# Kernel optimization log

Measured on AMD Instinct MI355X. Metric: run time of the kernel, lower is better.

Reference implementation:

```python
import jax, jax.numpy as jnp
import numpy as np


def setup_inputs() -> dict:
    key = jax.random.key(0)
    kq, kk, kv = jax.random.split(key, 3)
    B, N, M, H, D = 4, 2048, 2048, 8, 64
    queries = jax.random.normal(kq, (B, N, H, D), dtype=jnp.float32)
    keys = jax.random.normal(kk, (B, M, H, D), dtype=jnp.float32)
    values = jax.random.normal(kv, (B, M, H, D), dtype=jnp.float32)
    return {"queries": queries, "keys": keys, "values": values}


def reference(queries, keys, values):
    # queries: [B,N,H,D], keys/values: [B,M,H,D]
    D = queries.shape[3]
    softmax_temp = 1.0 / (D ** 0.5)
    QK = jnp.einsum('bnhd,bmhd->bnmh', queries, keys)  # [B,N,M,H]
    A = jax.nn.softmax(softmax_temp * QK, axis=2)      # softmax over M
    queried_values = jnp.einsum('bnmh,bmhd->bnhd', A, values)
    attention_weight = jnp.transpose(A, (0, 3, 1, 2))  # [B,H,N,M]
    return (queried_values, attention_weight)
```

## Files before the change

kernel.cpp:

```cpp
#include <hip/hip_runtime.h>

typedef __bf16 bf16x8 __attribute__((ext_vector_type(8)));
typedef float floatx4 __attribute__((ext_vector_type(4)));
typedef unsigned short ushort8 __attribute__((ext_vector_type(8)));
typedef unsigned short ushort4v __attribute__((ext_vector_type(4)));

#define MFMA(a, b, c) __builtin_amdgcn_mfma_f32_16x16x32_bf16((a), (b), (c), 0, 0, 0)

__device__ __forceinline__ unsigned short f2bf(float x) {
  union { float f; unsigned u; } v; v.f = x;
  unsigned r = v.u + 0x7FFFu + ((v.u >> 16) & 1u);
  return (unsigned short)(r >> 16);
}

__global__ __launch_bounds__(256)
void prep(const float* __restrict__ K, const float* __restrict__ V,
          unsigned short* __restrict__ Kb, unsigned short* __restrict__ Vt)
{
  int id = blockIdx.x * 256 + threadIdx.x;
  int isV = id >> 19;
  int cch = id & 524287;
  int bh = cch >> 14;
  int mt = (cch >> 9) & 31;
  int g  = cch & 511;
  int r  = g >> 3;
  int s  = g & 7;
  int e8 = s ^ (r & 7);
  int b = bh >> 3, h = bh & 7;
  ushort8 o;
  if (!isV) {
    const float* p = K + (((size_t)(b * 2048 + mt * 64 + r) * 8 + h) * 64 + e8 * 8);
    float4 x0 = *(const float4*)p;
    float4 x1 = *(const float4*)(p + 4);
    o[0] = f2bf(x0.x); o[1] = f2bf(x0.y); o[2] = f2bf(x0.z); o[3] = f2bf(x0.w);
    o[4] = f2bf(x1.x); o[5] = f2bf(x1.y); o[6] = f2bf(x1.z); o[7] = f2bf(x1.w);
    *(ushort8*)(Kb + (size_t)cch * 8) = o;
  } else {
    const float* p = V + (((size_t)(b * 2048 + mt * 64 + e8 * 8) * 8 + h) * 64 + r);
    #pragma unroll
    for (int j = 0; j < 8; ++j) o[j] = f2bf(p[(size_t)j * 512]);
    *(ushort8*)(Vt + (size_t)cch * 8) = o;
  }
}

__device__ __forceinline__ void stage2k(const unsigned short* gsrc, unsigned short* lds,
                                        int w, int l)
{
  const char* g = (const char*)gsrc + w * 2048 + l * 16;
  char* sd = (char*)lds + w * 2048;
  __builtin_amdgcn_global_load_lds((const __attribute__((address_space(1))) unsigned int*)g,
                                   (__attribute__((address_space(3))) unsigned int*)sd, 16, 0, 0);
  __builtin_amdgcn_global_load_lds((const __attribute__((address_space(1))) unsigned int*)(g + 1024),
                                   (__attribute__((address_space(3))) unsigned int*)(sd + 1024), 16, 0, 0);
}

__device__ __forceinline__ bf16x8 frag(const unsigned short* lds, int r, int bo)
{
  int slot = ((bo >> 4) ^ r) & 7;
  return *(const bf16x8*)((const char*)lds + r * 128 + (slot << 4));
}

__global__ __launch_bounds__(256, 4)
void attn_fwd(const float* __restrict__ Q, const unsigned short* __restrict__ Kb,
              const unsigned short* __restrict__ Vt,
              float* __restrict__ outQV, float* __restrict__ outA)
{
  __shared__ __align__(16) unsigned short Ks[2][4096];
  __shared__ __align__(16) unsigned short Vs[2][4096];
  __shared__ __align__(16) unsigned short As[4096];

  const int tid = threadIdx.x;
  const int w  = tid >> 6;
  const int l  = tid & 63;
  const int c  = l & 15;
  const int q4 = l >> 4;

  const int bx = blockIdx.x;
  const int qt = bx & 31;
  const int h  = (bx >> 5) & 7;
  const int b  = bx >> 8;
  const int q0 = qt * 64;

  const float scale = 0.125f * 1.44269504088896340736f;

  const size_t base = (size_t)b * (2048 * 512) + (size_t)h * 64;
  const float* Qb = Q + base + (size_t)q0 * 512;

  const unsigned short* Kt0 = Kb + (size_t)(b * 8 + h) * (32 * 4096);
  const unsigned short* Vt0 = Vt + (size_t)(b * 8 + h) * (32 * 4096);

  bf16x8 bQ0, bQ1;
  {
    const float* qp = Qb + (size_t)(16 * w + c) * 512 + q4 * 8;
    float4 qa0 = *(const float4*)(qp);
    float4 qa1 = *(const float4*)(qp + 4);
    float4 qb0 = *(const float4*)(qp + 32);
    float4 qb1 = *(const float4*)(qp + 36);
    ushort8 t0, t1;
    t0[0]=f2bf(qa0.x*scale); t0[1]=f2bf(qa0.y*scale); t0[2]=f2bf(qa0.z*scale); t0[3]=f2bf(qa0.w*scale);
    t0[4]=f2bf(qa1.x*scale); t0[5]=f2bf(qa1.y*scale); t0[6]=f2bf(qa1.z*scale); t0[7]=f2bf(qa1.w*scale);
    t1[0]=f2bf(qb0.x*scale); t1[1]=f2bf(qb0.y*scale); t1[2]=f2bf(qb0.z*scale); t1[3]=f2bf(qb0.w*scale);
    t1[4]=f2bf(qb1.x*scale); t1[5]=f2bf(qb1.y*scale); t1[6]=f2bf(qb1.z*scale); t1[7]=f2bf(qb1.w*scale);
    bQ0 = __builtin_bit_cast(bf16x8, t0);
    bQ1 = __builtin_bit_cast(bf16x8, t1);
  }

  stage2k(Kt0, Ks[0], w, l);
  float lsum[4] = {0.f, 0.f, 0.f, 0.f};
  int cur = 0;
  for (int mt = 0; mt < 32; ++mt) {
    __syncthreads();
    if (mt + 1 < 32) stage2k(Kt0 + (size_t)(mt + 1) * 4096, Ks[cur ^ 1], w, l);
    const unsigned short* Kc = Ks[cur];
    #pragma unroll
    for (int t = 0; t < 4; ++t) {
      bf16x8 aK0 = frag(Kc, t * 16 + c, q4 * 16);
      bf16x8 aK1 = frag(Kc, t * 16 + c, 64 + q4 * 16);
      floatx4 acc = {0.f, 0.f, 0.f, 0.f};
      acc = MFMA(aK0, bQ0, acc);
      acc = MFMA(aK1, bQ1, acc);
      #pragma unroll
      for (int i = 0; i < 4; ++i) lsum[i] += __builtin_amdgcn_exp2f(acc[i]);
    }
    cur ^= 1;
  }
  float rs = (lsum[0] + lsum[1]) + (lsum[2] + lsum[3]);
  rs += __shfl_xor(rs, 16);
  rs += __shfl_xor(rs, 32);
  const float rcp = 1.0f / rs;

  floatx4 Oacc[4];
  #pragma unroll
  for (int t = 0; t < 4; ++t) Oacc[t] = (floatx4){0.f, 0.f, 0.f, 0.f};

  const int arow = 16 * w + c;
  float* aRowP = outA + (((size_t)(b * 8 + h) * 2048 + q0 + arow) * 2048) + q4 * 4;

  __syncthreads();
  stage2k(Kt0, Ks[0], w, l);
  stage2k(Vt0, Vs[0], w, l);
  cur = 0;
  for (int mt = 0; mt < 32; ++mt) {
    __syncthreads();
    if (mt + 1 < 32) {
      stage2k(Kt0 + (size_t)(mt + 1) * 4096, Ks[cur ^ 1], w, l);
      stage2k(Vt0 + (size_t)(mt + 1) * 4096, Vs[cur ^ 1], w, l);
    }
    const unsigned short* Kc = Ks[cur];
    const unsigned short* Vc = Vs[cur];
    const int mc = mt * 64;
    #pragma unroll
    for (int t = 0; t < 4; ++t) {
      bf16x8 aK0 = frag(Kc, t * 16 + c, q4 * 16);
      bf16x8 aK1 = frag(Kc, t * 16 + c, 64 + q4 * 16);
      floatx4 acc = {0.f, 0.f, 0.f, 0.f};
      acc = MFMA(aK0, bQ0, acc);
      acc = MFMA(aK1, bQ1, acc);
      floatx4 av;
      av[0] = __builtin_amdgcn_exp2f(acc[0]) * rcp;
      av[1] = __builtin_amdgcn_exp2f(acc[1]) * rcp;
      av[2] = __builtin_amdgcn_exp2f(acc[2]) * rcp;
      av[3] = __builtin_amdgcn_exp2f(acc[3]) * rcp;
      __builtin_nontemporal_store(av, (floatx4*)(aRowP + mc + t * 16));
      ushort4v us = { f2bf(av[0]), f2bf(av[1]), f2bf(av[2]), f2bf(av[3]) };
      int bo = t * 32 + q4 * 8;
      int slot = ((bo >> 4) ^ arow) & 7;
      *(ushort4v*)((char*)As + arow * 128 + (slot << 4) + (bo & 15)) = us;
    }
    bf16x8 aP0 = frag(As, arow, q4 * 16);
    bf16x8 aP1 = frag(As, arow, 64 + q4 * 16);
    #pragma unroll
    for (int t = 0; t < 4; ++t) {
      bf16x8 bV0 = frag(Vc, t * 16 + c, q4 * 16);
      bf16x8 bV1 = frag(Vc, t * 16 + c, 64 + q4 * 16);
      Oacc[t] = MFMA(aP0, bV0, Oacc[t]);
      Oacc[t] = MFMA(aP1, bV1, Oacc[t]);
    }
    cur ^= 1;
  }

  #pragma unroll
  for (int t = 0; t < 4; ++t) {
    #pragma unroll
    for (int i = 0; i < 4; ++i) {
      outQV[base + (size_t)(q0 + 16 * w + q4 * 4 + i) * 512 + t * 16 + c] = Oacc[t][i];
    }
  }
}

extern "C" void kernel_launch(void* const* d_in, const int* in_sizes, int n_in,
                              void* d_out, int out_size, void* d_ws, size_t ws_size,
                              hipStream_t stream)
{
  const float* Q = (const float*)d_in[0];
  const float* K = (const float*)d_in[1];
  const float* V = (const float*)d_in[2];
  float* outQV = (float*)d_out;
  float* outA  = (float*)d_out + 4194304;

  unsigned short* Kb = (unsigned short*)d_ws;
  unsigned short* Vt = (unsigned short*)d_ws + 4194304;

  prep<<<dim3(4096), dim3(256), 0, stream>>>(K, V, Kb, Vt);
  attn_fwd<<<dim3(1024), dim3(256), 0, stream>>>(Q, Kb, Vt, outQV, outA);
}
```

Baseline: 656.2 us.

## Read K/V fragments straight from global memory and remap blocks for XCD locality

```diff
diff --git a/kernel.cpp b/kernel.cpp
--- a/kernel.cpp
+++ b/kernel.cpp
@@ -25,39 +25,26 @@
   int g  = cch & 511;
   int r  = g >> 3;
   int s  = g & 7;
-  int e8 = s ^ (r & 7);
   int b = bh >> 3, h = bh & 7;
   ushort8 o;
   if (!isV) {
-    const float* p = K + (((size_t)(b * 2048 + mt * 64 + r) * 8 + h) * 64 + e8 * 8);
+    const float* p = K + (((size_t)(b * 2048 + mt * 64 + r) * 8 + h) * 64 + s * 8);
     float4 x0 = *(const float4*)p;
     float4 x1 = *(const float4*)(p + 4);
     o[0] = f2bf(x0.x); o[1] = f2bf(x0.y); o[2] = f2bf(x0.z); o[3] = f2bf(x0.w);
     o[4] = f2bf(x1.x); o[5] = f2bf(x1.y); o[6] = f2bf(x1.z); o[7] = f2bf(x1.w);
     *(ushort8*)(Kb + (size_t)cch * 8) = o;
   } else {
-    const float* p = V + (((size_t)(b * 2048 + mt * 64 + e8 * 8) * 8 + h) * 64 + r);
+    const float* p = V + (((size_t)(b * 2048 + mt * 64 + s * 8) * 8 + h) * 64 + r);
     #pragma unroll
     for (int j = 0; j < 8; ++j) o[j] = f2bf(p[(size_t)j * 512]);
     *(ushort8*)(Vt + (size_t)cch * 8) = o;
   }
 }
 
-__device__ __forceinline__ void stage2k(const unsigned short* gsrc, unsigned short* lds,
-                                        int w, int l)
+__device__ __forceinline__ bf16x8 gfrag(const unsigned short* tile, int r, int e)
 {
-  const char* g = (const char*)gsrc + w * 2048 + l * 16;
-  char* sd = (char*)lds + w * 2048;
-  __builtin_amdgcn_global_load_lds((const __attribute__((address_space(1))) unsigned int*)g,
-                                   (__attribute__((address_space(3))) unsigned int*)sd, 16, 0, 0);
-  __builtin_amdgcn_global_load_lds((const __attribute__((address_space(1))) unsigned int*)(g + 1024),
-                                   (__attribute__((address_space(3))) unsigned int*)(sd + 1024), 16, 0, 0);
-}
-
-__device__ __forceinline__ bf16x8 frag(const unsigned short* lds, int r, int bo)
-{
-  int slot = ((bo >> 4) ^ r) & 7;
-  return *(const bf16x8*)((const char*)lds + r * 128 + (slot << 4));
+  return *(const bf16x8*)(tile + r * 64 + e);
 }
 
 __global__ __launch_bounds__(256, 4)
@@ -65,8 +52,6 @@
               const unsigned short* __restrict__ Vt,
               float* __restrict__ outQV, float* __restrict__ outA)
 {
-  __shared__ __align__(16) unsigned short Ks[2][4096];
-  __shared__ __align__(16) unsigned short Vs[2][4096];
   __shared__ __align__(16) unsigned short As[4096];
 
   const int tid = threadIdx.x;
@@ -75,7 +60,7 @@
   const int c  = l & 15;
   const int q4 = l >> 4;
 
-  const int bx = blockIdx.x;
+  const int bx = (blockIdx.x & 7) * 128 + (blockIdx.x >> 3);
   const int qt = bx & 31;
   const int h  = (bx >> 5) & 7;
   const int b  = bx >> 8;
@@ -105,24 +90,19 @@
     bQ1 = __builtin_bit_cast(bf16x8, t1);
   }
 
-  stage2k(Kt0, Ks[0], w, l);
   float lsum[4] = {0.f, 0.f, 0.f, 0.f};
-  int cur = 0;
   for (int mt = 0; mt < 32; ++mt) {
-    __syncthreads();
-    if (mt + 1 < 32) stage2k(Kt0 + (size_t)(mt + 1) * 4096, Ks[cur ^ 1], w, l);
-    const unsigned short* Kc = Ks[cur];
+    const unsigned short* gK = Kt0 + (size_t)mt * 4096;
     #pragma unroll
     for (int t = 0; t < 4; ++t) {
-      bf16x8 aK0 = frag(Kc, t * 16 + c, q4 * 16);
-      bf16x8 aK1 = frag(Kc, t * 16 + c, 64 + q4 * 16);
+      bf16x8 aK0 = gfrag(gK, t * 16 + c, q4 * 8);
+      bf16x8 aK1 = gfrag(gK, t * 16 + c, 32 + q4 * 8);
       floatx4 acc = {0.f, 0.f, 0.f, 0.f};
       acc = MFMA(aK0, bQ0, acc);
       acc = MFMA(aK1, bQ1, acc);
       #pragma unroll
       for (int i = 0; i < 4; ++i) lsum[i] += __builtin_amdgcn_exp2f(acc[i]);
     }
-    cur ^= 1;
   }
   float rs = (lsum[0] + lsum[1]) + (lsum[2] + lsum[3]);
   rs += __shfl_xor(rs, 16);
@@ -136,23 +116,14 @@
   const int arow = 16 * w + c;
   float* aRowP = outA + (((size_t)(b * 8 + h) * 2048 + q0 + arow) * 2048) + q4 * 4;
 
-  __syncthreads();
-  stage2k(Kt0, Ks[0], w, l);
-  stage2k(Vt0, Vs[0], w, l);
-  cur = 0;
   for (int mt = 0; mt < 32; ++mt) {
-    __syncthreads();
-    if (mt + 1 < 32) {
-      stage2k(Kt0 + (size_t)(mt + 1) * 4096, Ks[cur ^ 1], w, l);
-      stage2k(Vt0 + (size_t)(mt + 1) * 4096, Vs[cur ^ 1], w, l);
-    }
-    const unsigned short* Kc = Ks[cur];
-    const unsigned short* Vc = Vs[cur];
+    const unsigned short* gK = Kt0 + (size_t)mt * 4096;
+    const unsigned short* gV = Vt0 + (size_t)mt * 4096;
     const int mc = mt * 64;
     #pragma unroll
     for (int t = 0; t < 4; ++t) {
-      bf16x8 aK0 = frag(Kc, t * 16 + c, q4 * 16);
-      bf16x8 aK1 = frag(Kc, t * 16 + c, 64 + q4 * 16);
+      bf16x8 aK0 = gfrag(gK, t * 16 + c, q4 * 8);
+      bf16x8 aK1 = gfrag(gK, t * 16 + c, 32 + q4 * 8);
       floatx4 acc = {0.f, 0.f, 0.f, 0.f};
       acc = MFMA(aK0, bQ0, acc);
       acc = MFMA(aK1, bQ1, acc);
@@ -161,22 +132,25 @@
       av[1] = __builtin_amdgcn_exp2f(acc[1]) * rcp;
       av[2] = __builtin_amdgcn_exp2f(acc[2]) * rcp;
       av[3] = __builtin_amdgcn_exp2f(acc[3]) * rcp;
-      __builtin_nontemporal_store(av, (floatx4*)(aRowP + mc + t * 16));
+      *(floatx4*)(aRowP + mc + t * 16) = av;
       ushort4v us = { f2bf(av[0]), f2bf(av[1]), f2bf(av[2]), f2bf(av[3]) };
       int bo = t * 32 + q4 * 8;
       int slot = ((bo >> 4) ^ arow) & 7;
       *(ushort4v*)((char*)As + arow * 128 + (slot << 4) + (bo & 15)) = us;
     }
-    bf16x8 aP0 = frag(As, arow, q4 * 16);
-    bf16x8 aP1 = frag(As, arow, 64 + q4 * 16);
-    #pragma unroll
-    for (int t = 0; t < 4; ++t) {
-      bf16x8 bV0 = frag(Vc, t * 16 + c, q4 * 16);
-      bf16x8 bV1 = frag(Vc, t * 16 + c, 64 + q4 * 16);
-      Oacc[t] = MFMA(aP0, bV0, Oacc[t]);
-      Oacc[t] = MFMA(aP1, bV1, Oacc[t]);
+    {
+      int s0 = (((q4 * 16) >> 4) ^ arow) & 7;
+      int s1 = (((64 + q4 * 16) >> 4) ^ arow) & 7;
+      bf16x8 aP0 = *(const bf16x8*)((const char*)As + arow * 128 + (s0 << 4));
+      bf16x8 aP1 = *(const bf16x8*)((const char*)As + arow * 128 + (s1 << 4));
+      #pragma unroll
+      for (int t = 0; t < 4; ++t) {
+        bf16x8 bV0 = gfrag(gV, t * 16 + c, q4 * 8);
+        bf16x8 bV1 = gfrag(gV, t * 16 + c, 32 + q4 * 8);
+        Oacc[t] = MFMA(aP0, bV0, Oacc[t]);
+        Oacc[t] = MFMA(aP1, bV1, Oacc[t]);
+      }
     }
-    cur ^= 1;
   }
 
   #pragma unroll
```

After: 864.9 us. +31.8%, slower.
